# Optimization experiments

Measured on AMD Instinct MI355X. Metric: run time of the kernel, lower is better.

The kernel has to match this reference:

```python
import jax, jax.numpy as jnp
import numpy as np

N = 50000      # nodes
E = 800000     # edges
D_IN = 128     # irreps_in dim
SH = 16        # irreps_sh dim (lmax=3)
EA = 16        # edge_attr_dim
H = 8          # num_heads
DQ = 64        # irreps_query dim (8 per head)
DK = 64        # irreps_key dim (8 per head)
DV = 128       # irreps_out dim (16 per head)
HID = 64       # radial MLP hidden


def setup_inputs() -> dict:
    key = jax.random.key(0)
    ks = jax.random.split(key, 20)
    g = lambda k, shape, fan: jax.random.normal(k, shape, jnp.float32) / np.sqrt(fan)
    return {
        "node_attr": jax.random.normal(ks[0], (N, D_IN), jnp.float32),
        "edge_attr": jax.random.normal(ks[1], (E, EA), jnp.float32),
        "edge_sh": jax.random.normal(ks[2], (E, SH), jnp.float32),
        # h_q linear
        "Wq": g(ks[3], (D_IN, DQ), D_IN),
        # h_k conv: depthwise SH mixing, channel-mixing linear, radial MLP gate
        "Wang_k": g(ks[4], (D_IN, SH), SH),
        "Wlin_k": g(ks[5], (D_IN, DK), D_IN),
        "W1k": g(ks[6], (EA, HID), EA),
        "b1k": jnp.zeros((HID,), jnp.float32),
        "W2k": g(ks[7], (HID, DK), HID),
        # h_v conv
        "Wang_v": g(ks[8], (D_IN, SH), SH),
        "Wlin_v": g(ks[9], (D_IN, DV), D_IN),
        "W1v": g(ks[10], (EA, HID), EA),
        "b1v": jnp.zeros((HID,), jnp.float32),
        "W2v": g(ks[11], (HID, DV), HID),
        # FullyConnectedTensorProduct(query_per_head, key_per_head, '0e') -> weighted bilinear dot
        "Wdot": g(ks[12], (DQ // H, DK // H), DQ // H),
        # lin_out
        "Wout": g(ks[13], (DV, DV), DV),
        "edge_index": jax.random.randint(ks[14], (2, E), 0, N, jnp.int64),
    }


def _conv_per_edge(x_src, edge_attr, edge_sh, Wang, Wlin, W1, b1, W2):
    # depthwise tensor product of node feats with edge SH, channel mix, radial gate
    rad = jax.nn.relu(edge_attr @ W1 + b1) @ W2          # [E, Dout]
    g = edge_sh @ Wang.T                                  # [E, D_IN]
    return ((x_src * g) @ Wlin) * rad                     # [E, Dout]


def reference(node_attr, edge_attr, edge_sh, Wq, Wang_k, Wlin_k, W1k, b1k, W2k,
              Wang_v, Wlin_v, W1v, b1v, W2v, Wdot, Wout, edge_index):
    src, dst = edge_index[0], edge_index[1]
    n = node_attr.shape[0]
    e = src.shape[0]

    q = (node_attr @ Wq).reshape(n, H, DQ // H)           # [N,H,dq]
    x_src = node_attr[src]                                # gather [E,D_IN]
    k = _conv_per_edge(x_src, edge_attr, edge_sh, Wang_k, Wlin_k, W1k, b1k, W2k).reshape(e, H, DK // H)
    v = _conv_per_edge(x_src, edge_attr, edge_sh, Wang_v, Wlin_v, W1v, b1v, W2v).reshape(e, H, DV // H)

    # TP 'dot' to scalars: weighted bilinear per head
    alpha = jnp.einsum('ehq,qk,ehk->eh', q[dst], Wdot, k)  # [E,H]

    # scatter_softmax over incoming edges of each dst node
    amax = jax.ops.segment_max(alpha, dst, num_segments=n)  # [N,H]
    ealpha = jnp.exp(alpha - amax[dst])
    denom = jax.ops.segment_sum(ealpha, dst, num_segments=n)
    attn = ealpha / denom[dst]                              # [E,H]

    # weighted scatter-sum of values
    out = jax.ops.segment_sum(attn[..., None] * v, dst, num_segments=n)  # [N,H,dv]
    return out.reshape(n, DV) @ Wout
```

## Files before the change

kernel.cpp:

```cpp
#include <hip/hip_runtime.h>
#include <stdint.h>

#define NN 50000
#define NE 800000
#define STRIP 49

typedef unsigned int u32;
typedef uint16_t u16;

__device__ __forceinline__ float b2f(u16 u){ return __builtin_bit_cast(float, (u32)((u32)u << 16)); }
__device__ __forceinline__ float b2f_lo(u32 p){ return __builtin_bit_cast(float, p << 16); }
__device__ __forceinline__ float b2f_hi(u32 p){ return __builtin_bit_cast(float, p & 0xffff0000u); }
__device__ __forceinline__ u32 f2b_bits(float f){ u32 u = __builtin_bit_cast(u32, f); return (u + 0x7fffu + ((u >> 16) & 1u)) >> 16; }
__device__ __forceinline__ u16 f2b(float f){ return (u16)f2b_bits(f); }
__device__ __forceinline__ u32 packb(float lo, float hi){
  u32 r;
  asm("v_cvt_pk_bf16_f32 %0, %1, %2" : "=v"(r) : "v"(lo), "v"(hi));
  return r;
}

typedef __bf16 bf16x2 __attribute__((ext_vector_type(2)));
#if defined(__has_builtin)
#if __has_builtin(__builtin_amdgcn_fdot2_f32_bf16)
#define HAVE_DOT2_BUILTIN 1
#endif
#endif

#ifdef HAVE_DOT2_BUILTIN
__device__ __forceinline__ float dot2b(u32 a, u32 b, float c){
  return __builtin_amdgcn_fdot2_f32_bf16(__builtin_bit_cast(bf16x2, a),
                                         __builtin_bit_cast(bf16x2, b), c, false);
}
#else
__device__ __forceinline__ float dot2b(u32 a, u32 b, float c){
  c = fmaf(b2f_lo(a), b2f_lo(b), c);
  return fmaf(b2f_hi(a), b2f_hi(b), c);
}
#endif

typedef __attribute__((ext_vector_type(8))) short short8;
typedef __attribute__((ext_vector_type(4))) float f32x4;
__device__ __forceinline__ f32x4 mf32(uint4 a, uint4 b, f32x4 c){
  return __builtin_amdgcn_mfma_f32_16x16x32_bf16(
      __builtin_bit_cast(short8, a), __builtin_bit_cast(short8, b), c, 0, 0, 0);
}

__device__ __forceinline__ int chperm(int n){
  return 32 * ((n & 63) >> 4) + 8 * ((n & 15) >> 2) + 4 * (n >> 6) + (n & 3);
}

#define OFF_WANG_V 0
#define OFF_W1_V   5120
#define OFF_WLIN_V 7680
#define OFF_W2_V   25088
#define OFF_WANG_K 34304
#define OFF_W1_K   39424
#define OFF_WLIN_K 41984
#define OFF_W2_K   50688
#define OFF_WOUT   55296
#define OFF_WQD    72704
#define WT_TOTAL   81408

__global__ __launch_bounds__(256) void zero_kernel(int* __restrict__ counts,
                                                   int* __restrict__ edge_ids)
{
  int i = blockIdx.x * 256 + threadIdx.x;
  if (i < NN) counts[i] = 0;
  if (i < NE) edge_ids[i] = 0;
}

__global__ __launch_bounds__(256) void prep_w_kernel(
    const float* __restrict__ Wang_v, const float* __restrict__ W1_v,
    const float* __restrict__ Wlin_v, const float* __restrict__ W2_v,
    const float* __restrict__ Wang_k, const float* __restrict__ W1_k,
    const float* __restrict__ Wlin_k, const float* __restrict__ W2_k,
    const float* __restrict__ Wout, const float* __restrict__ Wq,
    const float* __restrict__ Wdot,
    u16* __restrict__ wt)
{
  int idx = blockIdx.x * 256 + threadIdx.x;
  if (idx >= WT_TOTAL) return;
  float val = 0.f;
  if (idx < OFF_W1_V) {
    int l = idx - OFF_WANG_V, n = l / 40, k = l % 40;
    if (k >= 16 && k < 32) val = Wang_v[chperm(n) * 16 + (k - 16)];
  } else if (idx < OFF_WLIN_V) {
    int l = idx - OFF_W1_V, n = l / 40, k = l % 40;
    if (k < 16) val = W1_v[k * 64 + n];
  } else if (idx < OFF_W2_V) {
    int l = idx - OFF_WLIN_V, n = l / 136, k = l % 136;
    if (k < 128) val = Wlin_v[k * 128 + chperm(n)];
  } else if (idx < OFF_WANG_K) {
    int l = idx - OFF_W2_V, n = l / 72, k = l % 72;
    if (k < 64) val = W2_v[k * 128 + chperm(n)];
  } else if (idx < OFF_W1_K) {
    int l = idx - OFF_WANG_K, n = l / 40, k = l % 40;
    if (k >= 16 && k < 32) val = Wang_k[chperm(n) * 16 + (k - 16)];
  } else if (idx < OFF_WLIN_K) {
    int l = idx - OFF_W1_K, n = l / 40, k = l % 40;
    if (k < 16) val = W1_k[k * 64 + n];
  } else if (idx < OFF_W2_K) {
    int l = idx - OFF_WLIN_K, n = l / 136, k = l % 136;
    if (k < 128) val = Wlin_k[k * 64 + n];
  } else if (idx < OFF_WOUT) {
    int l = idx - OFF_W2_K, n = l / 72, k = l % 72;
    if (k < 64) val = W2_k[k * 64 + n];
  } else if (idx < OFF_WQD) {
    int l = idx - OFF_WOUT, n = l / 136, k = l % 136;
    if (k < 128) val = Wout[k * 128 + n];
  } else {
    int l = idx - OFF_WQD, n = l / 136, k = l % 136;
    if (k < 128) {
      int h = n >> 3, r = n & 7;
      float s = 0.f;
#pragma unroll
      for (int i = 0; i < 8; ++i) s += Wq[k * 64 + h * 8 + i] * Wdot[i * 8 + r];
      val = s;
    }
  }
  wt[idx] = f2b(val);
}

__global__ __launch_bounds__(256) void qw_kernel(const float* __restrict__ node_attr,
                                                 const u16* __restrict__ wt,
                                                 u16* __restrict__ qw)
{
  __shared__ __align__(16) u16 sX[64 * 136];
  uint4* sX4 = (uint4*)sX;
  u32* sX32 = (u32*)sX;
  const uint4* wt4 = (const uint4*)wt;
  const int tid = threadIdx.x, wv = tid >> 6, lane = tid & 63, lq = lane >> 4, ln = lane & 15;
  const int n0 = blockIdx.x * 64;
  uint4 rB[4];
#pragma unroll
  for (int ks = 0; ks < 4; ++ks) rB[ks] = wt4[9088 + (wv * 16 + ln) * 17 + ks * 4 + lq];
  {
    int row = tid >> 2, q4 = tid & 3;
    int n = n0 + row;
    bool valid = n < NN;
    const float4* xp = (const float4*)(node_attr + (size_t)(valid ? n : 0) * 128);
#pragma unroll
    for (int i = 0; i < 8; ++i) {
      float4 v = valid ? xp[q4 * 8 + i] : make_float4(0.f, 0.f, 0.f, 0.f);
      sX32[row * 68 + (q4 * 8 + i) * 2]     = packb(v.x, v.y);
      sX32[row * 68 + (q4 * 8 + i) * 2 + 1] = packb(v.z, v.w);
    }
  }
  __syncthreads();
  const f32x4 z4 = {0.f, 0.f, 0.f, 0.f};
  int col = wv * 16 + ln;
#pragma unroll
  for (int et = 0; et < 4; ++et) {
    f32x4 acc = z4;
#pragma unroll
    for (int ks = 0; ks < 4; ++ks) acc = mf32(sX4[(et * 16 + ln) * 17 + ks * 4 + lq], rB[ks], acc);
#pragma unroll
    for (int r = 0; r < 4; ++r) {
      int rr = n0 + et * 16 + lq * 4 + r;
      if (rr < NN) qw[(size_t)rr * 64 + col] = f2b(acc[r]);
    }
  }
}

__global__ __launch_bounds__(256, 2) void conv_fused_kernel(
    const float* __restrict__ node_attr, const float* __restrict__ edge_attr,
    const float* __restrict__ edge_sh, const int* __restrict__ edge_index,
    const float* __restrict__ b1v, const float* __restrict__ b1k,
    const u16* __restrict__ wt, const u16* __restrict__ qw,
    u16* __restrict__ v_out, float* __restrict__ alpha)
{
  __shared__ __align__(16) u16 sC[64 * 40];
  __shared__ __align__(16) u16 sX[64 * 136];
  __shared__ __align__(16) u16 sTk[64 * 136];
  __shared__ __align__(16) u16 sHv[64 * 72];
  __shared__ __align__(16) u16 sHk[64 * 72];
  uint4* sC4 = (uint4*)sC; u32* sC32 = (u32*)sC;
  uint4* sX4 = (uint4*)sX;
  uint4* sTk4 = (uint4*)sTk;
  uint4* sHv4 = (uint4*)sHv;
  uint4* sHk4 = (uint4*)sHk;
  const uint4* wt4 = (const uint4*)wt;

  const int tid = threadIdx.x;
  const int wv = tid >> 6, lane = tid & 63, lq = lane >> 4, ln = lane & 15;
  const int e0 = blockIdx.x * 64;
  const int nA = wv * 16 + ln, nB = (wv + 4) * 16 + ln;
  const int cb  = wv * 16 + 4 * lq;
  const int cb8 = wv * 32 + 8 * lq;

  const int el = tid >> 2, p = tid & 3;
  int dq = edge_index[NE + e0 + el]; if ((u32)dq >= NN) dq = 0;
  const uint4* qptr = (const uint4*)(qw + (size_t)dq * 64 + p * 16);
  uint4 q0 = qptr[0], q1 = qptr[1];

  int srcs[4];
#pragma unroll
  for (int et = 0; et < 4; ++et) {
    int s = edge_index[e0 + et * 16 + ln];
    if ((u32)s >= NN) s = 0;
    srcs[et] = s;
  }

  uint4 rW1V    = wt4[640 + nA * 5 + lq];
  uint4 rW1K    = wt4[4928 + nA * 5 + lq];
  uint4 rWangV0 = wt4[nA * 5 + lq],        rWangV1 = wt4[nB * 5 + lq];
  uint4 rWangK0 = wt4[4288 + nA * 5 + lq], rWangK1 = wt4[4288 + nB * 5 + lq];
  float4 bV = *(const float4*)(b1v + cb);
  float4 bK = *(const float4*)(b1k + cb);

  {
    int r = tid >> 2, kq = tid & 3;
    float4 ea = ((const float4*)(edge_attr + (size_t)(e0 + r) * 16))[kq];
    *(uint2*)(sC32 + r * 20 + kq * 2) = make_uint2(packb(ea.x, ea.y), packb(ea.z, ea.w));
    float4 sh = ((const float4*)(edge_sh + (size_t)(e0 + r) * 16))[kq];
    *(uint2*)(sC32 + r * 20 + 8 + kq * 2) = make_uint2(packb(sh.x, sh.y), packb(sh.z, sh.w));
  }
  const float* xp0 = node_attr + (size_t)srcs[0] * 128 + cb8;
  float4 xa = *(const float4*)xp0;
  float4 xb = *(const float4*)(xp0 + 4);
  __syncthreads();

  const f32x4 z4 = {0.f, 0.f, 0.f, 0.f};
#pragma unroll
  for (int et = 0; et < 4; ++et) {
    float4 xa_n, xb_n;
    if (et < 3) {
      const float* xp = node_attr + (size_t)srcs[et + 1] * 128 + cb8;
      xa_n = *(const float4*)xp;
      xb_n = *(const float4*)(xp + 4);
    }
    uint4 aC = sC4[(et * 16 + ln) * 5 + lq];
    f32x4 hv  = mf32(rW1V, aC, z4);
    f32x4 hk  = mf32(rW1K, aC, z4);
    f32x4 t0v = mf32(rWangV0, aC, z4);
    f32x4 t1v = mf32(rWangV1, aC, z4);
    f32x4 t0k = mf32(rWangK0, aC, z4);
    f32x4 t1k = mf32(rWangK1, aC, z4);
    const int edge = et * 16 + ln;
    sX4[edge * 17 + 4 * wv + lq] = make_uint4(
        packb(t0v[0] * xa.x, t0v[1] * xa.y), packb(t0v[2] * xa.z, t0v[3] * xa.w),
        packb(t1v[0] * xb.x, t1v[1] * xb.y), packb(t1v[2] * xb.z, t1v[3] * xb.w));
    sTk4[edge * 17 + 4 * wv + lq] = make_uint4(
        packb(t0k[0] * xa.x, t0k[1] * xa.y), packb(t0k[2] * xa.z, t0k[3] * xa.w),
        packb(t1k[0] * xb.x, t1k[1] * xb.y), packb(t1k[2] * xb.z, t1k[3] * xb.w));
    *(uint2*)(sHv + edge * 72 + cb) = make_uint2(
        packb(fmaxf(hv[0] + bV.x, 0.f), fmaxf(hv[1] + bV.y, 0.f)),
        packb(fmaxf(hv[2] + bV.z, 0.f), fmaxf(hv[3] + bV.w, 0.f)));
    *(uint2*)(sHk + edge * 72 + cb) = make_uint2(
        packb(fmaxf(hk[0] + bK.x, 0.f), fmaxf(hk[1] + bK.y, 0.f)),
        packb(fmaxf(hk[2] + bK.z, 0.f), fmaxf(hk[3] + bK.w, 0.f)));
    xa = xa_n; xb = xb_n;
  }

  uint4 rWlinV[2][4], rWlinK[4], rW2V[2][2], rW2K[2];
#pragma unroll
  for (int ks = 0; ks < 4; ++ks) {
    rWlinV[0][ks] = wt4[960 + nA * 17 + ks * 4 + lq];
    rWlinV[1][ks] = wt4[960 + nB * 17 + ks * 4 + lq];
    rWlinK[ks]    = wt4[5248 + nA * 17 + ks * 4 + lq];
  }
#pragma unroll
  for (int ks = 0; ks < 2; ++ks) {
    rW2V[0][ks] = wt4[3136 + nA * 9 + ks * 4 + lq];
    rW2V[1][ks] = wt4[3136 + nB * 9 + ks * 4 + lq];
    rW2K[ks]    = wt4[6336 + nA * 9 + ks * 4 + lq];
  }
  __syncthreads();

  uint4 pv[4]; uint2 pk[4];
#pragma unroll
  for (int et = 0; et < 4; ++et) {
    const int er = et * 16 + ln;
    f32x4 acc0 = z4, acc1 = z4, acck = z4;
#pragma unroll
    for (int ks = 0; ks < 4; ++ks) {
      uint4 tb = sX4[er * 17 + ks * 4 + lq];
      acc0 = mf32(rWlinV[0][ks], tb, acc0);
      acc1 = mf32(rWlinV[1][ks], tb, acc1);
      acck = mf32(rWlinK[ks], sTk4[er * 17 + ks * 4 + lq], acck);
    }
    f32x4 b0 = z4, b1 = z4, bk = z4;
#pragma unroll
    for (int ks = 0; ks < 2; ++ks) {
      uint4 hb = sHv4[er * 9 + ks * 4 + lq];
      b0 = mf32(rW2V[0][ks], hb, b0);
      b1 = mf32(rW2V[1][ks], hb, b1);
      bk = mf32(rW2K[ks], sHk4[er * 9 + ks * 4 + lq], bk);
    }
    pv[et] = make_uint4(packb(acc0[0] * b0[0], acc0[1] * b0[1]),
                        packb(acc0[2] * b0[2], acc0[3] * b0[3]),
                        packb(acc1[0] * b1[0], acc1[1] * b1[1]),
                        packb(acc1[2] * b1[2], acc1[3] * b1[3]));
    pk[et] = make_uint2(packb(acck[0] * bk[0], acck[1] * bk[1]),
                        packb(acck[2] * bk[2], acck[3] * bk[3]));
  }
  __syncthreads();

#pragma unroll
  for (int et = 0; et < 4; ++et) {
    const int edge = et * 16 + ln;
    sX4[edge * 17 + 4 * wv + lq] = pv[et];
    *(uint2*)(sHk + edge * 72 + cb) = pk[et];
  }
  __syncthreads();

  {
    int row = tid >> 2, seg = tid & 3;
    uint4* gp = (uint4*)(v_out + (size_t)(e0 + row) * 128);
#pragma unroll
    for (int i = 0; i < 4; ++i) gp[seg * 4 + i] = sX4[row * 17 + seg * 4 + i];
  }
  {
    uint4 k0 = sHk4[el * 9 + p * 2];
    uint4 k1 = sHk4[el * 9 + p * 2 + 1];
    float a0 = 0.f, a1 = 0.f;
    a0 = dot2b(q0.x, k0.x, a0); a0 = dot2b(q0.y, k0.y, a0);
    a0 = dot2b(q0.z, k0.z, a0); a0 = dot2b(q0.w, k0.w, a0);
    a1 = dot2b(q1.x, k1.x, a1); a1 = dot2b(q1.y, k1.y, a1);
    a1 = dot2b(q1.z, k1.z, a1); a1 = dot2b(q1.w, k1.w, a1);
    ((float2*)(alpha + (size_t)(e0 + el) * 8))[p] = make_float2(a0, a1);
  }
}

__global__ __launch_bounds__(256) void count_kernel(const int* __restrict__ edge_index,
                                                    int* __restrict__ counts)
{
  int e = blockIdx.x * 256 + threadIdx.x;
  if (e < NE) { int d = edge_index[NE + e]; if ((u32)d >= NN) d = 0; atomicAdd(&counts[d], 1); }
}

__global__ __launch_bounds__(1024) void scan_kernel(const int* __restrict__ counts,
                                                    int* __restrict__ row_ptr,
                                                    int* __restrict__ cursor)
{
  __shared__ int s[1024];
  int tid = threadIdx.x;
  int base = tid * STRIP;
  int sum = 0;
  for (int i = 0; i < STRIP; ++i) { int idx = base + i; sum += (idx < NN) ? counts[idx] : 0; }
  s[tid] = sum;
  __syncthreads();
  for (int off = 1; off < 1024; off <<= 1) {
    int v = s[tid];
    int add = (tid >= off) ? s[tid - off] : 0;
    __syncthreads();
    s[tid] = v + add;
    __syncthreads();
  }
  int running = (tid == 0) ? 0 : s[tid - 1];
  for (int i = 0; i < STRIP; ++i) {
    int idx = base + i;
    if (idx < NN) { row_ptr[idx] = running; cursor[idx] = running; running += counts[idx]; }
  }
  if (tid == 1023) row_ptr[NN] = running;
}

__global__ __launch_bounds__(256) void fill_kernel(const int* __restrict__ edge_index,
                                                   int* __restrict__ cursor,
                                                   int* __restrict__ edge_ids)
{
  int e = blockIdx.x * 256 + threadIdx.x;
  if (e < NE) {
    int dst = edge_index[NE + e]; if ((u32)dst >= NN) dst = 0;
    int pos = atomicAdd(&cursor[dst], 1);
    if ((u32)pos < NE) edge_ids[pos] = e;
  }
}

#define OUPD(aa, ww)                                                   \
  { float mn = fmaxf(m, (aa));                                         \
    float sc = __expf(m - mn);                                         \
    float pw = __expf((aa) - mn);                                      \
    l = l * sc + pw;                                                   \
    accA = accA * sc + pw * b2f_lo(ww);                                \
    accB = accB * sc + pw * b2f_hi(ww);                                \
    m = mn; }

__global__ __launch_bounds__(256) void out_kernel(
    const int* __restrict__ row_ptr, const int* __restrict__ edge_ids,
    const float* __restrict__ alpha, const u16* __restrict__ v_e,
    const u16* __restrict__ wt, float* __restrict__ out)
{
  __shared__ __align__(16) u16 sAgg[16 * 136];
  u32* sAgg32 = (u32*)sAgg;
  uint4* sAgg4 = (uint4*)sAgg;
  const uint4* wt4 = (const uint4*)wt;
  const u32* v32 = (const u32*)v_e;
  const int tid = threadIdx.x, wv = tid >> 6, lane = tid & 63, lq = lane >> 4, ln = lane & 15;
  const f32x4 z4 = {0.f, 0.f, 0.f, 0.f};
  uint4 rWT[2][4];
#pragma unroll
  for (int c = 0; c < 2; ++c) {
    int n = (wv * 2 + c) * 16 + ln;
#pragma unroll
    for (int ks = 0; ks < 4; ++ks) rWT[c][ks] = wt4[6912 + n * 17 + ks * 4 + lq];
  }
  const int hh = lane >> 3;
  const int grp = blockIdx.x;
#pragma unroll 1
  for (int i = 0; i < 4; ++i) {
    int n = grp * 16 + wv * 4 + i;
    int beg = row_ptr[n], end = row_ptr[n + 1];
    if (beg < 0) beg = 0; if (beg > NE) beg = NE;
    if (end < beg) end = beg; if (end > NE) end = NE;
    int deg = end - beg;
    float m = -3.0e38f, l = 0.f, accA = 0.f, accB = 0.f;
    int j = 0;
#pragma unroll 1
    for (; j + 4 <= deg; j += 4) {
      int e0 = edge_ids[beg + j],     e1 = edge_ids[beg + j + 1];
      int e2 = edge_ids[beg + j + 2], e3 = edge_ids[beg + j + 3];
      if ((u32)e0 >= NE) e0 = 0; if ((u32)e1 >= NE) e1 = 0;
      if ((u32)e2 >= NE) e2 = 0; if ((u32)e3 >= NE) e3 = 0;
      float a0 = alpha[(size_t)e0 * 8 + hh]; u32 w0 = v32[(size_t)e0 * 64 + lane];
      float a1 = alpha[(size_t)e1 * 8 + hh]; u32 w1 = v32[(size_t)e1 * 64 + lane];
      float a2 = alpha[(size_t)e2 * 8 + hh]; u32 w2 = v32[(size_t)e2 * 64 + lane];
      float a3 = alpha[(size_t)e3 * 8 + hh]; u32 w3 = v32[(size_t)e3 * 64 + lane];
      OUPD(a0, w0); OUPD(a1, w1); OUPD(a2, w2); OUPD(a3, w3);
    }
#pragma unroll 1
    for (; j < deg; ++j) {
      int e = edge_ids[beg + j]; if ((u32)e >= NE) e = 0;
      float a = alpha[(size_t)e * 8 + hh]; u32 w = v32[(size_t)e * 64 + lane];
      OUPD(a, w);
    }
    float inv = (l > 0.f) ? (1.f / l) : 0.f;
    accA *= inv; accB *= inv;
    sAgg32[(wv * 4 + i) * 68 + lane] = packb(accA, accB);
  }
  __syncthreads();
#pragma unroll
  for (int c = 0; c < 2; ++c) {
    f32x4 acc = z4;
#pragma unroll
    for (int ks = 0; ks < 4; ++ks) acc = mf32(sAgg4[ln * 17 + ks * 4 + lq], rWT[c][ks], acc);
    int col = (wv * 2 + c) * 16 + ln;
#pragma unroll
    for (int r = 0; r < 4; ++r)
      out[(size_t)(grp * 16 + lq * 4 + r) * 128 + col] = acc[r];
  }
}

extern "C" void kernel_launch(void* const* d_in, const int* in_sizes, int n_in,
                              void* d_out, int out_size, void* d_ws, size_t ws_size,
                              hipStream_t stream)
{
  const float* node_attr = (const float*)d_in[0];
  const float* edge_attr = (const float*)d_in[1];
  const float* edge_sh   = (const float*)d_in[2];
  const float* Wq        = (const float*)d_in[3];
  const float* Wang_k    = (const float*)d_in[4];
  const float* Wlin_k    = (const float*)d_in[5];
  const float* W1k       = (const float*)d_in[6];
  const float* b1k       = (const float*)d_in[7];
  const float* W2k       = (const float*)d_in[8];
  const float* Wang_v    = (const float*)d_in[9];
  const float* Wlin_v    = (const float*)d_in[10];
  const float* W1v       = (const float*)d_in[11];
  const float* b1v       = (const float*)d_in[12];
  const float* W2v       = (const float*)d_in[13];
  const float* Wdot      = (const float*)d_in[14];
  const float* Wout      = (const float*)d_in[15];
  const int* edge_index  = (const int*)d_in[16];
  float* out = (float*)d_out;

  char* ws = (char*)d_ws;
  u16*   v_e      = (u16*)(ws + 0);
  float* alpha    = (float*)(ws + 204800000);
  u16*   qw       = (u16*)(ws + 230400000);
  int*   counts   = (int*)(ws + 236800000);
  int*   row_ptr  = (int*)(ws + 237000064);
  int*   cursor   = (int*)(ws + 237200128);
  int*   edge_ids = (int*)(ws + 237400192);
  u16*   wt       = (u16*)(ws + 240600192);

  zero_kernel<<<dim3((NE + 255) / 256), dim3(256), 0, stream>>>(counts, edge_ids);
  prep_w_kernel<<<dim3((WT_TOTAL + 255) / 256), dim3(256), 0, stream>>>(
      Wang_v, W1v, Wlin_v, W2v, Wang_k, W1k, Wlin_k, W2k, Wout, Wq, Wdot, wt);
  qw_kernel<<<dim3((NN + 63) / 64), dim3(256), 0, stream>>>(node_attr, wt, qw);
  conv_fused_kernel<<<dim3(NE / 64), dim3(256), 0, stream>>>(
      node_attr, edge_attr, edge_sh, edge_index, b1v, b1k, wt, qw, v_e, alpha);
  count_kernel<<<dim3((NE + 255) / 256), dim3(256), 0, stream>>>(edge_index, counts);
  scan_kernel<<<dim3(1), dim3(1024), 0, stream>>>(counts, row_ptr, cursor);
  fill_kernel<<<dim3((NE + 255) / 256), dim3(256), 0, stream>>>(edge_index, cursor, edge_ids);
  out_kernel<<<dim3(3125), dim3(256), 0, stream>>>(row_ptr, edge_ids, alpha, v_e, wt, out);
}
```

Baseline: 680.9 us.

## Scatter per-edge values and logits into dst-sorted order inside conv kernel

The CSR build (count, scan, fill) now runs before the conv kernel, and fill records each edge's sorted position instead of a sorted edge-id list. The conv kernel writes v and alpha directly to that dst-sorted slot, so out_kernel reads contiguous rows without the indirection through edge_ids. The zero kernel also shrinks to clearing only the counts array. In exchange, the conv kernel's stores become scattered rows rather than coalesced blocks, and the CSR stages now sit on the critical path before conv.

```diff
diff --git a/kernel.cpp b/kernel.cpp
--- a/kernel.cpp
+++ b/kernel.cpp
@@ -61,12 +61,10 @@
 #define OFF_WQD    72704
 #define WT_TOTAL   81408
 
-__global__ __launch_bounds__(256) void zero_kernel(int* __restrict__ counts,
-                                                   int* __restrict__ edge_ids)
+__global__ __launch_bounds__(256) void zero_kernel(int* __restrict__ counts)
 {
   int i = blockIdx.x * 256 + threadIdx.x;
   if (i < NN) counts[i] = 0;
-  if (i < NE) edge_ids[i] = 0;
 }
 
 __global__ __launch_bounds__(256) void prep_w_kernel(
@@ -162,11 +160,57 @@
   }
 }
 
+__global__ __launch_bounds__(256) void count_kernel(const int* __restrict__ edge_index,
+                                                    int* __restrict__ counts)
+{
+  int e = blockIdx.x * 256 + threadIdx.x;
+  if (e < NE) { int d = edge_index[NE + e]; if ((u32)d >= NN) d = 0; atomicAdd(&counts[d], 1); }
+}
+
+__global__ __launch_bounds__(1024) void scan_kernel(const int* __restrict__ counts,
+                                                    int* __restrict__ row_ptr,
+                                                    int* __restrict__ cursor)
+{
+  __shared__ int s[1024];
+  int tid = threadIdx.x;
+  int base = tid * STRIP;
+  int sum = 0;
+  for (int i = 0; i < STRIP; ++i) { int idx = base + i; sum += (idx < NN) ? counts[idx] : 0; }
+  s[tid] = sum;
+  __syncthreads();
+  for (int off = 1; off < 1024; off <<= 1) {
+    int v = s[tid];
+    int add = (tid >= off) ? s[tid - off] : 0;
+    __syncthreads();
+    s[tid] = v + add;
+    __syncthreads();
+  }
+  int running = (tid == 0) ? 0 : s[tid - 1];
+  for (int i = 0; i < STRIP; ++i) {
+    int idx = base + i;
+    if (idx < NN) { row_ptr[idx] = running; cursor[idx] = running; running += counts[idx]; }
+  }
+  if (tid == 1023) row_ptr[NN] = running;
+}
+
+__global__ __launch_bounds__(256) void fill_kernel(const int* __restrict__ edge_index,
+                                                   int* __restrict__ cursor,
+                                                   int* __restrict__ edge_pos)
+{
+  int e = blockIdx.x * 256 + threadIdx.x;
+  if (e < NE) {
+    int dst = edge_index[NE + e]; if ((u32)dst >= NN) dst = 0;
+    int pos = atomicAdd(&cursor[dst], 1);
+    edge_pos[e] = ((u32)pos < NE) ? pos : 0;
+  }
+}
+
 __global__ __launch_bounds__(256, 2) void conv_fused_kernel(
     const float* __restrict__ node_attr, const float* __restrict__ edge_attr,
     const float* __restrict__ edge_sh, const int* __restrict__ edge_index,
     const float* __restrict__ b1v, const float* __restrict__ b1k,
     const u16* __restrict__ wt, const u16* __restrict__ qw,
+    const int* __restrict__ edge_pos,
     u16* __restrict__ v_out, float* __restrict__ alpha)
 {
   __shared__ __align__(16) u16 sC[64 * 40];
@@ -192,6 +236,7 @@
   int dq = edge_index[NE + e0 + el]; if ((u32)dq >= NN) dq = 0;
   const uint4* qptr = (const uint4*)(qw + (size_t)dq * 64 + p * 16);
   uint4 q0 = qptr[0], q1 = qptr[1];
+  int pos_el = edge_pos[e0 + el]; if ((u32)pos_el >= NE) pos_el = 0;
 
   int srcs[4];
 #pragma unroll
@@ -306,7 +351,7 @@
 
   {
     int row = tid >> 2, seg = tid & 3;
-    uint4* gp = (uint4*)(v_out + (size_t)(e0 + row) * 128);
+    uint4* gp = (uint4*)(v_out + (size_t)pos_el * 128);
 #pragma unroll
     for (int i = 0; i < 4; ++i) gp[seg * 4 + i] = sX4[row * 17 + seg * 4 + i];
   }
@@ -318,52 +363,7 @@
     a0 = dot2b(q0.z, k0.z, a0); a0 = dot2b(q0.w, k0.w, a0);
     a1 = dot2b(q1.x, k1.x, a1); a1 = dot2b(q1.y, k1.y, a1);
     a1 = dot2b(q1.z, k1.z, a1); a1 = dot2b(q1.w, k1.w, a1);
-    ((float2*)(alpha + (size_t)(e0 + el) * 8))[p] = make_float2(a0, a1);
-  }
-}
-
-__global__ __launch_bounds__(256) void count_kernel(const int* __restrict__ edge_index,
-                                                    int* __restrict__ counts)
-{
-  int e = blockIdx.x * 256 + threadIdx.x;
-  if (e < NE) { int d = edge_index[NE + e]; if ((u32)d >= NN) d = 0; atomicAdd(&counts[d], 1); }
-}
-
-__global__ __launch_bounds__(1024) void scan_kernel(const int* __restrict__ counts,
-                                                    int* __restrict__ row_ptr,
-                                                    int* __restrict__ cursor)
-{
-  __shared__ int s[1024];
-  int tid = threadIdx.x;
-  int base = tid * STRIP;
-  int sum = 0;
-  for (int i = 0; i < STRIP; ++i) { int idx = base + i; sum += (idx < NN) ? counts[idx] : 0; }
-  s[tid] = sum;
-  __syncthreads();
-  for (int off = 1; off < 1024; off <<= 1) {
-    int v = s[tid];
-    int add = (tid >= off) ? s[tid - off] : 0;
-    __syncthreads();
-    s[tid] = v + add;
-    __syncthreads();
-  }
-  int running = (tid == 0) ? 0 : s[tid - 1];
-  for (int i = 0; i < STRIP; ++i) {
-    int idx = base + i;
-    if (idx < NN) { row_ptr[idx] = running; cursor[idx] = running; running += counts[idx]; }
-  }
-  if (tid == 1023) row_ptr[NN] = running;
-}
-
-__global__ __launch_bounds__(256) void fill_kernel(const int* __restrict__ edge_index,
-                                                   int* __restrict__ cursor,
-                                                   int* __restrict__ edge_ids)
-{
-  int e = blockIdx.x * 256 + threadIdx.x;
-  if (e < NE) {
-    int dst = edge_index[NE + e]; if ((u32)dst >= NN) dst = 0;
-    int pos = atomicAdd(&cursor[dst], 1);
-    if ((u32)pos < NE) edge_ids[pos] = e;
+    ((float2*)(alpha + (size_t)pos_el * 8))[p] = make_float2(a0, a1);
   }
 }
 
@@ -377,7 +377,7 @@
     m = mn; }
 
 __global__ __launch_bounds__(256) void out_kernel(
-    const int* __restrict__ row_ptr, const int* __restrict__ edge_ids,
+    const int* __restrict__ row_ptr,
     const float* __restrict__ alpha, const u16* __restrict__ v_e,
     const u16* __restrict__ wt, float* __restrict__ out)
 {
@@ -408,20 +408,17 @@
     int j = 0;
 #pragma unroll 1
     for (; j + 4 <= deg; j += 4) {
-      int e0 = edge_ids[beg + j],     e1 = edge_ids[beg + j + 1];
-      int e2 = edge_ids[beg + j + 2], e3 = edge_ids[beg + j + 3];
-      if ((u32)e0 >= NE) e0 = 0; if ((u32)e1 >= NE) e1 = 0;
-      if ((u32)e2 >= NE) e2 = 0; if ((u32)e3 >= NE) e3 = 0;
-      float a0 = alpha[(size_t)e0 * 8 + hh]; u32 w0 = v32[(size_t)e0 * 64 + lane];
-      float a1 = alpha[(size_t)e1 * 8 + hh]; u32 w1 = v32[(size_t)e1 * 64 + lane];
-      float a2 = alpha[(size_t)e2 * 8 + hh]; u32 w2 = v32[(size_t)e2 * 64 + lane];
-      float a3 = alpha[(size_t)e3 * 8 + hh]; u32 w3 = v32[(size_t)e3 * 64 + lane];
+      size_t b = (size_t)(beg + j);
+      float a0 = alpha[(b)     * 8 + hh]; u32 w0 = v32[(b)     * 64 + lane];
+      float a1 = alpha[(b + 1) * 8 + hh]; u32 w1 = v32[(b + 1) * 64 + lane];
+      float a2 = alpha[(b + 2) * 8 + hh]; u32 w2 = v32[(b + 2) * 64 + lane];
+      float a3 = alpha[(b + 3) * 8 + hh]; u32 w3 = v32[(b + 3) * 64 + lane];
       OUPD(a0, w0); OUPD(a1, w1); OUPD(a2, w2); OUPD(a3, w3);
     }
 #pragma unroll 1
     for (; j < deg; ++j) {
-      int e = edge_ids[beg + j]; if ((u32)e >= NE) e = 0;
-      float a = alpha[(size_t)e * 8 + hh]; u32 w = v32[(size_t)e * 64 + lane];
+      size_t b = (size_t)(beg + j);
+      float a = alpha[b * 8 + hh]; u32 w = v32[b * 64 + lane];
       OUPD(a, w);
     }
     float inv = (l > 0.f) ? (1.f / l) : 0.f;
@@ -471,17 +468,17 @@
   int*   counts   = (int*)(ws + 236800000);
   int*   row_ptr  = (int*)(ws + 237000064);
   int*   cursor   = (int*)(ws + 237200128);
-  int*   edge_ids = (int*)(ws + 237400192);
+  int*   edge_pos = (int*)(ws + 237400192);
   u16*   wt       = (u16*)(ws + 240600192);
 
-  zero_kernel<<<dim3((NE + 255) / 256), dim3(256), 0, stream>>>(counts, edge_ids);
+  zero_kernel<<<dim3((NN + 255) / 256), dim3(256), 0, stream>>>(counts);
   prep_w_kernel<<<dim3((WT_TOTAL + 255) / 256), dim3(256), 0, stream>>>(
       Wang_v, W1v, Wlin_v, W2v, Wang_k, W1k, Wlin_k, W2k, Wout, Wq, Wdot, wt);
   qw_kernel<<<dim3((NN + 63) / 64), dim3(256), 0, stream>>>(node_attr, wt, qw);
-  conv_fused_kernel<<<dim3(NE / 64), dim3(256), 0, stream>>>(
-      node_attr, edge_attr, edge_sh, edge_index, b1v, b1k, wt, qw, v_e, alpha);
   count_kernel<<<dim3((NE + 255) / 256), dim3(256), 0, stream>>>(edge_index, counts);
   scan_kernel<<<dim3(1), dim3(1024), 0, stream>>>(counts, row_ptr, cursor);
-  fill_kernel<<<dim3((NE + 255) / 256), dim3(256), 0, stream>>>(edge_index, cursor, edge_ids);
-  out_kernel<<<dim3(3125), dim3(256), 0, stream>>>(row_ptr, edge_ids, alpha, v_e, wt, out);
-}
+  fill_kernel<<<dim3((NE + 255) / 256), dim3(256), 0, stream>>>(edge_index, cursor, edge_pos);
+  conv_fused_kernel<<<dim3(NE / 64), dim3(256), 0, stream>>>(
+      node_attr, edge_attr, edge_sh, edge_index, b1v, b1k, wt, qw, edge_pos, v_e, alpha);
+  out_kernel<<<dim3(3125), dim3(256), 0, stream>>>(row_ptr, alpha, v_e, wt, out);
+}
```

Measured after the change: 642.6 us. -5.6%, faster.
